# Kernel optimization log

Hardware: AMD Instinct MI355X
Metric: run time of the kernel (lower is better)

Reference implementation:

```python
import jax, jax.numpy as jnp
import numpy as np

N = 50000      # nodes
E = 800000     # edges
IN = 256       # in_dim
H = 3          # num_heads
C = 64         # hidden_dim (per head)
D = H * C      # per-layer width = 192
OUT = 64       # out_dim
EPS_BN = 1e-5


def _gat_layer(h, W, att_src, att_dst, bias, src, dst):
    """PyG GATConv (concat=True, no self loops, eval/no dropout).
    h: [N, F_in], W: [F_in, H*C], att_src/att_dst: [H, C], bias: [H*C]."""
    x = (h @ W).reshape(-1, H, C)                       # [N, H, C]
    a_s = jnp.einsum('nhc,hc->nh', x, att_src)          # [N, H]
    a_d = jnp.einsum('nhc,hc->nh', x, att_dst)          # [N, H]
    e = jax.nn.leaky_relu(a_s[src] + a_d[dst], 0.2)     # [E, H]
    # segment softmax over incoming edges of each destination node
    m = jax.ops.segment_max(e, dst, num_segments=N)     # [N, H]
    m = jnp.where(jnp.isfinite(m), m, 0.0)
    w = jnp.exp(e - m[dst])                             # [E, H]
    den = jax.ops.segment_sum(w, dst, num_segments=N)   # [N, H]
    alpha = w / (den[dst] + 1e-16)                      # [E, H]
    out = jax.ops.segment_sum(x[src] * alpha[:, :, None], dst, num_segments=N)
    return out.reshape(-1, D) + bias                    # [N, H*C]


def _batchnorm(h, gamma, beta):
    mu = h.mean(0)
    var = h.var(0)
    return (h - mu) * jax.lax.rsqrt(var + EPS_BN) * gamma + beta


def setup_inputs() -> dict:
    key = jax.random.key(0)
    ks = jax.random.split(key, 16)
    s_in = 1.0 / np.sqrt(IN)
    s_d = 1.0 / np.sqrt(D)
    inp = {
        'x': jax.random.normal(ks[0], (N, IN), jnp.float32),
        'W1': jax.random.normal(ks[1], (IN, D), jnp.float32) * s_in,
        'att_src1': jax.random.normal(ks[2], (H, C), jnp.float32) * s_d,
        'att_dst1': jax.random.normal(ks[3], (H, C), jnp.float32) * s_d,
        'b1': jnp.zeros((D,), jnp.float32),
        'g1': jnp.ones((D,), jnp.float32),
        'beta1': jnp.zeros((D,), jnp.float32),
        'W2': jax.random.normal(ks[4], (D, D), jnp.float32) * s_d,
        'att_src2': jax.random.normal(ks[5], (H, C), jnp.float32) * s_d,
        'att_dst2': jax.random.normal(ks[6], (H, C), jnp.float32) * s_d,
        'b2': jnp.zeros((D,), jnp.float32),
        'g2': jnp.ones((D,), jnp.float32),
        'beta2': jnp.zeros((D,), jnp.float32),
        'Wf': jax.random.normal(ks[7], (D, OUT), jnp.float32) * s_d,
        'bf': jnp.zeros((OUT,), jnp.float32),
        'edge_index': jax.random.randint(ks[8], (2, E), 0, N, jnp.int64),
    }
    return inp


def reference(x, W1, att_src1, att_dst1, b1, g1, beta1,
              W2, att_src2, att_dst2, b2, g2, beta2,
              Wf, bf, edge_index):
    src, dst = edge_index[0], edge_index[1]
    h1 = _gat_layer(x, W1, att_src1, att_dst1, b1, src, dst)
    h1 = _batchnorm(jax.nn.relu(h1), g1, beta1)
    h2 = _gat_layer(h1, W2, att_src2, att_dst2, b2, src, dst)
    h2 = _batchnorm(jax.nn.relu(h2), g2, beta2)
    h_sum = h1 + h2
    return h_sum @ Wf + bf
```

## Files before the change

kernel.cpp:

```cpp
#include <hip/hip_runtime.h>

#define NN 50000
#define NE 800000
#define DIN 256
#define NH 3
#define HC 64
#define DD 192
#define DF 64
#define NB 196

typedef __attribute__((ext_vector_type(8))) short s8bf;
typedef __attribute__((ext_vector_type(8))) unsigned short u16x8;
typedef __attribute__((ext_vector_type(4))) float f32x4;

__device__ __forceinline__ unsigned short f2bf(float f) {
    unsigned u = __float_as_uint(f);
    unsigned r = u + 0x7fffu + ((u >> 16) & 1u);
    return (unsigned short)(r >> 16);
}
__device__ __forceinline__ float bf2f(unsigned short h) {
    return __uint_as_float(((unsigned)h) << 16);
}
__device__ __forceinline__ void split2(float f, unsigned short& h, unsigned short& l) {
    h = f2bf(f);
    l = f2bf(f - bf2f(h));
}
__device__ __forceinline__ float rl_f(float v, int j) {
    return __int_as_float(__builtin_amdgcn_readlane(__float_as_int(v), j));
}

#define W1G (DIN / 8 * DD)
#define W2G (DD / 8 * DD)
#define WFG (DD / 8 * DF)
__global__ __launch_bounds__(256)
void wsplit_all(const float* __restrict__ W1, const float* __restrict__ W2,
                const float* __restrict__ Wf,
                unsigned short* __restrict__ W1hT, unsigned short* __restrict__ W1lT,
                unsigned short* __restrict__ W2hT, unsigned short* __restrict__ W2lT,
                unsigned short* __restrict__ WfhT, unsigned short* __restrict__ WflT) {
    int idx = blockIdx.x * 256 + threadIdx.x;
    const float* W; unsigned short *Wh, *Wl; int K, D, base;
    if (idx < W1G)                  { W = W1; Wh = W1hT; Wl = W1lT; K = DIN; D = DD; base = idx; }
    else if (idx < W1G + W2G)       { W = W2; Wh = W2hT; Wl = W2lT; K = DD;  D = DD; base = idx - W1G; }
    else if (idx < W1G + W2G + WFG) { W = Wf; Wh = WfhT; Wl = WflT; K = DD;  D = DF; base = idx - W1G - W2G; }
    else return;
    int kb = base / D, d = base - kb * D;
    u16x8 hv, lv;
#pragma unroll
    for (int q = 0; q < 8; ++q) {
        unsigned short h, l;
        split2(W[(size_t)(kb * 8 + q) * D + d], h, l);
        hv[q] = h; lv[q] = l;
    }
    *(u16x8*)(Wh + (size_t)d * K + kb * 8) = hv;
    *(u16x8*)(Wl + (size_t)d * K + kb * 8) = lv;
}

__global__ void bn_fin(const float* __restrict__ s1, const float* __restrict__ s2,
                       const float* __restrict__ g, const float* __restrict__ beta,
                       float* __restrict__ scale, float* __restrict__ shift) {
    int j = threadIdx.x;
    const float invn = 1.0f / NN;
    float mu = s1[j] * invn;
    float var = s2[j] * invn - mu * mu;
    float sc = g[j] * rsqrtf(var + 1e-5f);
    scale[j] = sc;
    shift[j] = beta[j] - mu * sc;
}

template<int K, int DOUT, int MODE, bool DOTS>
__global__ __launch_bounds__(256)
void mfma_gemm(const float* __restrict__ A1, const float* __restrict__ A2,
               const float* __restrict__ bb1, const float* __restrict__ sc1,
               const float* __restrict__ sh1,
               const float* __restrict__ bb2, const float* __restrict__ sc2,
               const float* __restrict__ sh2,
               const unsigned short* __restrict__ BhT, const unsigned short* __restrict__ BlT,
               const float* __restrict__ att_s, const float* __restrict__ att_d,
               float4* __restrict__ as4o, float4* __restrict__ ad4o,
               const float* __restrict__ obias, float* __restrict__ Yf,
               unsigned short* __restrict__ Yb, int n) {
    constexpr int NT = DOUT / 64;
    constexpr int KB8 = K / 8;
    __shared__ unsigned short AH[64 * KB8 * 8];
    __shared__ float sdots[DOTS ? 4 : 1][64][6];

    const int tid = threadIdx.x;
    const int wave = tid >> 6, lane = tid & 63;
    const int r = lane & 15, kg = lane >> 4;
    const int row0 = blockIdx.x * 64;
    const int col0 = wave * (DOUT / 4);

    for (int idx = tid; idx < 64 * KB8; idx += 256) {
        int row = idx / KB8, kb = idx - row * KB8;
        int grow = min(row0 + row, n - 1);
        int j = kb * 8;
        const float* ap = A1 + (size_t)grow * K + j;
        float v[8];
        *(float4*)&v[0] = *(const float4*)ap;
        *(float4*)&v[4] = *(const float4*)(ap + 4);
        if constexpr (MODE >= 1) {
#pragma unroll
            for (int q = 0; q < 8; ++q)
                v[q] = fmaxf(v[q] + bb1[j + q], 0.f) * sc1[j + q] + sh1[j + q];
        }
        if constexpr (MODE == 2) {
            const float* ap2 = A2 + (size_t)grow * K + j;
            float u[8];
            *(float4*)&u[0] = *(const float4*)ap2;
            *(float4*)&u[4] = *(const float4*)(ap2 + 4);
#pragma unroll
            for (int q = 0; q < 8; ++q)
                v[q] += fmaxf(u[q] + bb2[j + q], 0.f) * sc2[j + q] + sh2[j + q];
        }
        u16x8 hv;
#pragma unroll
        for (int q = 0; q < 8; ++q)
            hv[q] = f2bf(v[q]);
        int sw = kb ^ (row & 7);
        *(u16x8*)&AH[(row * KB8 + sw) * 8] = hv;
    }
    __syncthreads();

    int boff[NT];
#pragma unroll
    for (int t = 0; t < NT; ++t)
        boff[t] = (col0 + t * 16 + r) * K + kg * 8;

    f32x4 acc[4][NT] = {};

    for (int k0 = 0; k0 < K; k0 += 32) {
        s8bf bh[NT], bl[NT];
#pragma unroll
        for (int t = 0; t < NT; ++t) {
            bh[t] = *(const s8bf*)(BhT + boff[t] + k0);
            bl[t] = *(const s8bf*)(BlT + boff[t] + k0);
        }
        const int kb = k0 / 8 + kg;
        s8bf ah[4];
#pragma unroll
        for (int g = 0; g < 4; ++g) {
            int row = g * 16 + r;
            int sw = kb ^ (row & 7);
            ah[g] = *(const s8bf*)&AH[(row * KB8 + sw) * 8];
        }
#pragma unroll
        for (int g = 0; g < 4; ++g)
#pragma unroll
            for (int t = 0; t < NT; ++t) {
                acc[g][t] = __builtin_amdgcn_mfma_f32_16x16x32_bf16(ah[g], bh[t], acc[g][t], 0, 0, 0);
                acc[g][t] = __builtin_amdgcn_mfma_f32_16x16x32_bf16(ah[g], bl[t], acc[g][t], 0, 0, 0);
            }
    }

#pragma unroll
    for (int t = 0; t < NT; ++t) {
        int col = col0 + t * 16 + r;
        float b = (MODE == 2) ? obias[col] : 0.f;
#pragma unroll
        for (int g = 0; g < 4; ++g) {
#pragma unroll
            for (int rr = 0; rr < 4; ++rr) {
                int row = row0 + g * 16 + kg * 4 + rr;
                if (row < n) {
                    if constexpr (MODE == 2)
                        Yf[(size_t)row * DOUT + col] = acc[g][t][rr] + b;
                    else
                        Yb[(size_t)row * DOUT + col] = f2bf(acc[g][t][rr]);
                }
            }
        }
    }

    if constexpr (DOTS) {
        float asv[NT], adv[NT];
        int headt[NT];
#pragma unroll
        for (int t = 0; t < NT; ++t) {
            int col = col0 + t * 16 + r;
            asv[t] = att_s[col];
            adv[t] = att_d[col];
            headt[t] = (col0 + t * 16) >> 6;
        }
#pragma unroll
        for (int g = 0; g < 4; ++g) {
#pragma unroll
            for (int rr = 0; rr < 4; ++rr) {
                float rs0 = 0.f, rs1 = 0.f, rs2 = 0.f;
                float rd0 = 0.f, rd1 = 0.f, rd2 = 0.f;
#pragma unroll
                for (int t = 0; t < NT; ++t) {
                    float v = acc[g][t][rr];
                    float s = v * asv[t], dd = v * adv[t];
                    if (headt[t] == 0)      { rs0 += s; rd0 += dd; }
                    else if (headt[t] == 1) { rs1 += s; rd1 += dd; }
                    else                    { rs2 += s; rd2 += dd; }
                }
#pragma unroll
                for (int m = 1; m < 16; m <<= 1) {
                    rs0 += __shfl_xor(rs0, m); rs1 += __shfl_xor(rs1, m); rs2 += __shfl_xor(rs2, m);
                    rd0 += __shfl_xor(rd0, m); rd1 += __shfl_xor(rd1, m); rd2 += __shfl_xor(rd2, m);
                }
                if (r == 0) {
                    int row = g * 16 + kg * 4 + rr;
                    sdots[wave][row][0] = rs0; sdots[wave][row][1] = rs1; sdots[wave][row][2] = rs2;
                    sdots[wave][row][3] = rd0; sdots[wave][row][4] = rd1; sdots[wave][row][5] = rd2;
                }
            }
        }
        __syncthreads();
        if (tid < 64) {
            int row = row0 + tid;
            if (row < n) {
                float s0 = 0.f, s1 = 0.f, s2 = 0.f, d0 = 0.f, d1 = 0.f, d2 = 0.f;
#pragma unroll
                for (int w = 0; w < 4; ++w) {
                    s0 += sdots[w][tid][0]; s1 += sdots[w][tid][1]; s2 += sdots[w][tid][2];
                    d0 += sdots[w][tid][3]; d1 += sdots[w][tid][4]; d2 += sdots[w][tid][5];
                }
                as4o[row] = make_float4(s0, s1, s2, 0.f);
                ad4o[row] = make_float4(d0, d1, d2, 0.f);
            }
        }
    }
}

__global__ void hist_kernel(const int* __restrict__ dst, int* __restrict__ deg, int ne) {
    int e = blockIdx.x * blockDim.x + threadIdx.x;
    if (e < ne) atomicAdd(&deg[dst[e]], 1);
}

__global__ __launch_bounds__(256)
void blocksum_kernel(const int* __restrict__ deg, int* __restrict__ bsum) {
    int i = blockIdx.x * 256 + threadIdx.x;
    int v = (i < NN) ? deg[i] : 0;
#pragma unroll
    for (int off = 32; off; off >>= 1) v += __shfl_down(v, off);
    __shared__ int ws[4];
    if ((threadIdx.x & 63) == 0) ws[threadIdx.x >> 6] = v;
    __syncthreads();
    if (threadIdx.x == 0) bsum[blockIdx.x] = ws[0] + ws[1] + ws[2] + ws[3];
}

__global__ __launch_bounds__(256)
void scan_bsums(const int* __restrict__ bsum, int* __restrict__ boff,
                int* __restrict__ rowptr) {
    __shared__ int s[256];
    int t = threadIdx.x;
    int v = (t < NB) ? bsum[t] : 0;
    s[t] = v;
    __syncthreads();
    for (int off = 1; off < 256; off <<= 1) {
        int u = (t >= off) ? s[t - off] : 0;
        __syncthreads();
        s[t] += u;
        __syncthreads();
    }
    if (t < NB) boff[t] = s[t] - v;
    if (t == 255) rowptr[NN] = s[255];
}

__global__ __launch_bounds__(256)
void expand_kernel(const int* __restrict__ deg, const int* __restrict__ boff,
                   int* __restrict__ rowptr, int* __restrict__ cursor) {
    __shared__ int s[256];
    int t = threadIdx.x;
    int i = blockIdx.x * 256 + t;
    int v = (i < NN) ? deg[i] : 0;
    s[t] = v;
    __syncthreads();
    for (int off = 1; off < 256; off <<= 1) {
        int u = (t >= off) ? s[t - off] : 0;
        __syncthreads();
        s[t] += u;
        __syncthreads();
    }
    if (i < NN) {
        int excl = s[t] - v + boff[blockIdx.x];
        rowptr[i] = excl;
        cursor[i] = excl;
    }
}

__global__ void scatter_kernel(const int* __restrict__ src, const int* __restrict__ dst,
                               int* __restrict__ cursor, int* __restrict__ csr_src, int ne) {
    int e = blockIdx.x * blockDim.x + threadIdx.x;
    if (e >= ne) return;
    int d = dst[e];
    int pos = atomicAdd(&cursor[d], 1);
    csr_src[pos] = src[e];
}

__global__ __launch_bounds__(256)
void gat_gather(const unsigned short* __restrict__ xf,
                const float4* __restrict__ as4, const float4* __restrict__ ad4,
                const int* __restrict__ rowptr, const int* __restrict__ csr_src,
                float* __restrict__ outp) {
    int d = blockIdx.x * 4 + (threadIdx.x >> 6);
    if (d >= NN) return;
    const int lane = threadIdx.x & 63;
    const int beg = rowptr[d], end = rowptr[d + 1];
    const float4 adv = ad4[d];

    float a0 = 0.f, a1 = 0.f, a2 = 0.f;
    float den0 = 0.f, den1 = 0.f, den2 = 0.f;

    for (int base = beg; base < end; base += 64) {
        const int nb = min(64, end - base);
        int sl = 0;
        float w0 = 0.f, w1 = 0.f, w2 = 0.f;
        if (lane < nb) {
            sl = csr_src[base + lane];
            float4 av = as4[sl];
            float e0 = av.x + adv.x;
            float e1 = av.y + adv.y;
            float e2 = av.z + adv.z;
            e0 = e0 > 0.f ? e0 : 0.2f * e0;
            e1 = e1 > 0.f ? e1 : 0.2f * e1;
            e2 = e2 > 0.f ? e2 : 0.2f * e2;
            w0 = __expf(e0); w1 = __expf(e1); w2 = __expf(e2);
        }
        float r0 = w0, r1 = w1, r2 = w2;
#pragma unroll
        for (int off = 1; off < 64; off <<= 1) {
            r0 += __shfl_xor(r0, off);
            r1 += __shfl_xor(r1, off);
            r2 += __shfl_xor(r2, off);
        }
        den0 += r0; den1 += r1; den2 += r2;

        int j = 0;
        for (; j + 8 <= nb; j += 8) {
            const unsigned short* xp[8];
            float uw0[8], uw1[8], uw2[8];
#pragma unroll
            for (int k = 0; k < 8; ++k) {
                int s = __builtin_amdgcn_readlane(sl, j + k);
                xp[k] = xf + (size_t)s * DD;
                uw0[k] = rl_f(w0, j + k);
                uw1[k] = rl_f(w1, j + k);
                uw2[k] = rl_f(w2, j + k);
            }
            unsigned short f0[8], f1[8], f2[8];
#pragma unroll
            for (int k = 0; k < 8; ++k) {
                f0[k] = xp[k][lane];
                f1[k] = xp[k][64 + lane];
                f2[k] = xp[k][128 + lane];
            }
#pragma unroll
            for (int k = 0; k < 8; ++k) {
                a0 = fmaf(bf2f(f0[k]), uw0[k], a0);
                a1 = fmaf(bf2f(f1[k]), uw1[k], a1);
                a2 = fmaf(bf2f(f2[k]), uw2[k], a2);
            }
        }
        for (; j < nb; ++j) {
            int s = __builtin_amdgcn_readlane(sl, j);
            float u0 = rl_f(w0, j), u1 = rl_f(w1, j), u2 = rl_f(w2, j);
            const unsigned short* xp = xf + (size_t)s * DD;
            a0 = fmaf(bf2f(xp[lane]),       u0, a0);
            a1 = fmaf(bf2f(xp[64 + lane]),  u1, a1);
            a2 = fmaf(bf2f(xp[128 + lane]), u2, a2);
        }
    }
    size_t o = (size_t)d * DD + lane;
    outp[o]       = a0 / (den0 + 1e-16f);
    outp[o + 64]  = a1 / (den1 + 1e-16f);
    outp[o + 128] = a2 / (den2 + 1e-16f);
}

__global__ __launch_bounds__(192)
void bn_stats(const float* __restrict__ hbuf, const float* __restrict__ bias,
              float* __restrict__ s1, float* __restrict__ s2, int n) {
    int j = threadIdx.x;
    float b = bias[j];
    int r0 = blockIdx.x * 64;
    int r1 = min(r0 + 64, n);
    float a = 0.f, q = 0.f;
    for (int r = r0; r < r1; ++r) {
        float v = hbuf[(size_t)r * DD + j] + b;
        v = fmaxf(v, 0.f);
        a += v; q += v * v;
    }
    atomicAdd(&s1[j], a);
    atomicAdd(&s2[j], q);
}

extern "C" void kernel_launch(void* const* d_in, const int* in_sizes, int n_in,
                              void* d_out, int out_size, void* d_ws, size_t ws_size,
                              hipStream_t stream) {
    const float* x   = (const float*)d_in[0];
    const float* W1  = (const float*)d_in[1];
    const float* as1 = (const float*)d_in[2];
    const float* ad1 = (const float*)d_in[3];
    const float* b1  = (const float*)d_in[4];
    const float* g1  = (const float*)d_in[5];
    const float* be1 = (const float*)d_in[6];
    const float* W2  = (const float*)d_in[7];
    const float* as2 = (const float*)d_in[8];
    const float* ad2 = (const float*)d_in[9];
    const float* b2  = (const float*)d_in[10];
    const float* g2  = (const float*)d_in[11];
    const float* be2 = (const float*)d_in[12];
    const float* Wf  = (const float*)d_in[13];
    const float* bf  = (const float*)d_in[14];
    const int*   ei  = (const int*)d_in[15];
    const int* src = ei;
    const int* dst = ei + NE;
    float* out = (float*)d_out;

    float* ws = (float*)d_ws;
    float* CB1 = ws;
    float* CB2 = CB1 + (size_t)NN * DD;
    float4* AS4 = (float4*)(CB2 + (size_t)NN * DD);
    float4* AD4 = AS4 + NN;
    int* DEG   = (int*)(AD4 + NN);
    float* S1a = (float*)(DEG + NN);
    float* S2a = S1a + DD;
    float* S1b = S2a + DD;
    float* S2b = S1b + DD;
    float* SC1 = S2b + DD;
    float* SH1 = SC1 + DD;
    float* SC2 = SH1 + DD;
    float* SH2 = SC2 + DD;
    int* ROWPTR = (int*)(SH2 + DD);
    int* CURSOR = ROWPTR + NN + 1;
    int* BSUM   = CURSOR + NN;
    int* BOFF   = BSUM + NB;
    int* CSRS   = BOFF + NB;
    unsigned short* R    = (unsigned short*)(CSRS + NE);
    unsigned short* Abf  = R;
    unsigned short* W1hT = Abf + (size_t)NN * DD;
    unsigned short* W1lT = W1hT + DIN * DD;
    unsigned short* W2hT = W1lT + DIN * DD;
    unsigned short* W2lT = W2hT + DD * DD;
    unsigned short* WfhT = W2lT + DD * DD;
    unsigned short* WflT = WfhT + DD * DF;

    const int edge_grid = (NE + 255) / 256;
    const int gemm_grid = (NN + 63) / 64;
    const int gat_grid  = (NN + 3) / 4;
    const int bns_grid  = (NN + 63) / 64;
    const int wsp_grid  = (W1G + W2G + WFG + 255) / 256;

    hipMemsetAsync(DEG, 0, (size_t)NN * 4 + 4 * DD * 4, stream);

    hist_kernel<<<edge_grid, 256, 0, stream>>>(dst, DEG, NE);
    blocksum_kernel<<<NB, 256, 0, stream>>>(DEG, BSUM);
    scan_bsums<<<1, 256, 0, stream>>>(BSUM, BOFF, ROWPTR);
    expand_kernel<<<NB, 256, 0, stream>>>(DEG, BOFF, ROWPTR, CURSOR);
    scatter_kernel<<<edge_grid, 256, 0, stream>>>(src, dst, CURSOR, CSRS, NE);

    wsplit_all<<<wsp_grid, 256, 0, stream>>>(W1, W2, Wf, W1hT, W1lT, W2hT, W2lT, WfhT, WflT);

    mfma_gemm<DIN, DD, 0, true><<<gemm_grid, 256, 0, stream>>>(
        x, nullptr,
        nullptr, nullptr, nullptr,
        nullptr, nullptr, nullptr,
        W1hT, W1lT, as1, ad1, AS4, AD4, nullptr, nullptr, Abf, NN);
    gat_gather<<<gat_grid, 256, 0, stream>>>(Abf, AS4, AD4, ROWPTR, CSRS, CB1);
    bn_stats<<<bns_grid, 192, 0, stream>>>(CB1, b1, S1a, S2a, NN);
    bn_fin<<<1, DD, 0, stream>>>(S1a, S2a, g1, be1, SC1, SH1);

    mfma_gemm<DD, DD, 1, true><<<gemm_grid, 256, 0, stream>>>(
        CB1, nullptr,
        b1, SC1, SH1,
        nullptr, nullptr, nullptr,
        W2hT, W2lT, as2, ad2, AS4, AD4, nullptr, nullptr, Abf, NN);
    gat_gather<<<gat_grid, 256, 0, stream>>>(Abf, AS4, AD4, ROWPTR, CSRS, CB2);
    bn_stats<<<bns_grid, 192, 0, stream>>>(CB2, b2, S1b, S2b, NN);
    bn_fin<<<1, DD, 0, stream>>>(S1b, S2b, g2, be2, SC2, SH2);

    mfma_gemm<DD, DF, 2, false><<<gemm_grid, 256, 0, stream>>>(
        CB1, CB2,
        b1, SC1, SH1,
        b2, SC2, SH2,
        WfhT, WflT, nullptr, nullptr, nullptr, nullptr, bf, out, nullptr, NN);
}
```

Baseline: 417.2 us.

## Fold BN finalize into GEMM prologue and software-pipeline A/B loads

Removes the two single-block bn_fin launches by having each GEMM block compute the batchnorm scale and shift from the raw sums into shared memory. The A-tile staging loop and the MFMA k-loop are software-pipelined so the next iteration's global and LDS loads are issued before the current compute. This cuts launch overhead and hides load latency, at the cost of redundant per-block BN math and higher register pressure.

```diff
diff --git a/kernel.cpp b/kernel.cpp
--- a/kernel.cpp
+++ b/kernel.cpp
@@ -56,25 +56,15 @@
     *(u16x8*)(Wl + (size_t)d * K + kb * 8) = lv;
 }
 
-__global__ void bn_fin(const float* __restrict__ s1, const float* __restrict__ s2,
-                       const float* __restrict__ g, const float* __restrict__ beta,
-                       float* __restrict__ scale, float* __restrict__ shift) {
-    int j = threadIdx.x;
-    const float invn = 1.0f / NN;
-    float mu = s1[j] * invn;
-    float var = s2[j] * invn - mu * mu;
-    float sc = g[j] * rsqrtf(var + 1e-5f);
-    scale[j] = sc;
-    shift[j] = beta[j] - mu * sc;
-}
-
 template<int K, int DOUT, int MODE, bool DOTS>
 __global__ __launch_bounds__(256)
 void mfma_gemm(const float* __restrict__ A1, const float* __restrict__ A2,
-               const float* __restrict__ bb1, const float* __restrict__ sc1,
-               const float* __restrict__ sh1,
-               const float* __restrict__ bb2, const float* __restrict__ sc2,
-               const float* __restrict__ sh2,
+               const float* __restrict__ bb1, const float* __restrict__ S1a_,
+               const float* __restrict__ S2a_, const float* __restrict__ g1_,
+               const float* __restrict__ be1_,
+               const float* __restrict__ bb2, const float* __restrict__ S1b_,
+               const float* __restrict__ S2b_, const float* __restrict__ g2_,
+               const float* __restrict__ be2_,
                const unsigned short* __restrict__ BhT, const unsigned short* __restrict__ BlT,
                const float* __restrict__ att_s, const float* __restrict__ att_d,
                float4* __restrict__ as4o, float4* __restrict__ ad4o,
@@ -82,8 +72,10 @@
                unsigned short* __restrict__ Yb, int n) {
     constexpr int NT = DOUT / 64;
     constexpr int KB8 = K / 8;
+    constexpr int NCF = (MODE == 2) ? 4 : (MODE == 1 ? 2 : 1);
     __shared__ unsigned short AH[64 * KB8 * 8];
     __shared__ float sdots[DOTS ? 4 : 1][64][6];
+    __shared__ float cf[NCF][DD];
 
     const int tid = threadIdx.x;
     const int wave = tid >> 6, lane = tid & 63;
@@ -91,27 +83,70 @@
     const int row0 = blockIdx.x * 64;
     const int col0 = wave * (DOUT / 4);
 
-    for (int idx = tid; idx < 64 * KB8; idx += 256) {
+    if constexpr (MODE >= 1) {
+        if (tid < DD) {
+            const float invn = 1.0f / NN;
+            float mu = S1a_[tid] * invn;
+            float var = S2a_[tid] * invn - mu * mu;
+            float sc = g1_[tid] * rsqrtf(var + 1e-5f);
+            cf[0][tid] = sc;
+            cf[1][tid] = be1_[tid] - mu * sc;
+            if constexpr (MODE == 2) {
+                mu = S1b_[tid] * invn;
+                var = S2b_[tid] * invn - mu * mu;
+                sc = g2_[tid] * rsqrtf(var + 1e-5f);
+                cf[2][tid] = sc;
+                cf[3][tid] = be2_[tid] - mu * sc;
+            }
+        }
+        __syncthreads();
+    }
+
+    constexpr int SIT = 64 * KB8 / 256;
+    auto aoff = [&](int i) {
+        int idx = tid + i * 256;
         int row = idx / KB8, kb = idx - row * KB8;
         int grow = min(row0 + row, n - 1);
+        return (size_t)grow * K + kb * 8;
+    };
+    float4 cv0, cv1, cu0, cu1;
+    {
+        size_t o0 = aoff(0);
+        cv0 = *(const float4*)(A1 + o0);
+        cv1 = *(const float4*)(A1 + o0 + 4);
+        if constexpr (MODE == 2) {
+            cu0 = *(const float4*)(A2 + o0);
+            cu1 = *(const float4*)(A2 + o0 + 4);
+        }
+    }
+#pragma unroll
+    for (int i = 0; i < SIT; ++i) {
+        float4 nv0, nv1, nu0, nu1;
+        if (i + 1 < SIT) {
+            size_t on = aoff(i + 1);
+            nv0 = *(const float4*)(A1 + on);
+            nv1 = *(const float4*)(A1 + on + 4);
+            if constexpr (MODE == 2) {
+                nu0 = *(const float4*)(A2 + on);
+                nu1 = *(const float4*)(A2 + on + 4);
+            }
+        }
+        int idx = tid + i * 256;
+        int row = idx / KB8, kb = idx - row * KB8;
         int j = kb * 8;
-        const float* ap = A1 + (size_t)grow * K + j;
         float v[8];
-        *(float4*)&v[0] = *(const float4*)ap;
-        *(float4*)&v[4] = *(const float4*)(ap + 4);
+        *(float4*)&v[0] = cv0; *(float4*)&v[4] = cv1;
         if constexpr (MODE >= 1) {
 #pragma unroll
             for (int q = 0; q < 8; ++q)
-                v[q] = fmaxf(v[q] + bb1[j + q], 0.f) * sc1[j + q] + sh1[j + q];
+                v[q] = fmaxf(v[q] + bb1[j + q], 0.f) * cf[0][j + q] + cf[1][j + q];
         }
         if constexpr (MODE == 2) {
-            const float* ap2 = A2 + (size_t)grow * K + j;
             float u[8];
-            *(float4*)&u[0] = *(const float4*)ap2;
-            *(float4*)&u[4] = *(const float4*)(ap2 + 4);
+            *(float4*)&u[0] = cu0; *(float4*)&u[4] = cu1;
 #pragma unroll
             for (int q = 0; q < 8; ++q)
-                v[q] += fmaxf(u[q] + bb2[j + q], 0.f) * sc2[j + q] + sh2[j + q];
+                v[q] += fmaxf(u[q] + bb2[j + q], 0.f) * cf[2][j + q] + cf[3][j + q];
         }
         u16x8 hv;
 #pragma unroll
@@ -119,6 +154,8 @@
             hv[q] = f2bf(v[q]);
         int sw = kb ^ (row & 7);
         *(u16x8*)&AH[(row * KB8 + sw) * 8] = hv;
+        cv0 = nv0; cv1 = nv1;
+        if constexpr (MODE == 2) { cu0 = nu0; cu1 = nu1; }
     }
     __syncthreads();
 
@@ -129,28 +166,44 @@
 
     f32x4 acc[4][NT] = {};
 
-    for (int k0 = 0; k0 < K; k0 += 32) {
-        s8bf bh[NT], bl[NT];
+    auto loadB = [&](int k0, s8bf* bh, s8bf* bl) {
 #pragma unroll
         for (int t = 0; t < NT; ++t) {
             bh[t] = *(const s8bf*)(BhT + boff[t] + k0);
             bl[t] = *(const s8bf*)(BlT + boff[t] + k0);
         }
+    };
+    auto loadA = [&](int k0, s8bf* ah) {
         const int kb = k0 / 8 + kg;
-        s8bf ah[4];
 #pragma unroll
         for (int g = 0; g < 4; ++g) {
             int row = g * 16 + r;
             int sw = kb ^ (row & 7);
             ah[g] = *(const s8bf*)&AH[(row * KB8 + sw) * 8];
         }
+    };
+
+    s8bf bh[NT], bl[NT], ah4[4];
+    loadB(0, bh, bl);
+    loadA(0, ah4);
+#pragma unroll
+    for (int k0 = 0; k0 < K; k0 += 32) {
+        s8bf nbh[NT], nbl[NT], nah[4];
+        if (k0 + 32 < K) {
+            loadB(k0 + 32, nbh, nbl);
+            loadA(k0 + 32, nah);
+        }
 #pragma unroll
         for (int g = 0; g < 4; ++g)
 #pragma unroll
             for (int t = 0; t < NT; ++t) {
-                acc[g][t] = __builtin_amdgcn_mfma_f32_16x16x32_bf16(ah[g], bh[t], acc[g][t], 0, 0, 0);
-                acc[g][t] = __builtin_amdgcn_mfma_f32_16x16x32_bf16(ah[g], bl[t], acc[g][t], 0, 0, 0);
-            }
+                acc[g][t] = __builtin_amdgcn_mfma_f32_16x16x32_bf16(ah4[g], bh[t], acc[g][t], 0, 0, 0);
+                acc[g][t] = __builtin_amdgcn_mfma_f32_16x16x32_bf16(ah4[g], bl[t], acc[g][t], 0, 0, 0);
+            }
+#pragma unroll
+        for (int t = 0; t < NT; ++t) { bh[t] = nbh[t]; bl[t] = nbl[t]; }
+#pragma unroll
+        for (int g = 0; g < 4; ++g) ah4[g] = nah[g];
     }
 
 #pragma unroll
@@ -456,25 +509,23 @@
 
     mfma_gemm<DIN, DD, 0, true><<<gemm_grid, 256, 0, stream>>>(
         x, nullptr,
-        nullptr, nullptr, nullptr,
-        nullptr, nullptr, nullptr,
+        nullptr, nullptr, nullptr, nullptr, nullptr,
+        nullptr, nullptr, nullptr, nullptr, nullptr,
         W1hT, W1lT, as1, ad1, AS4, AD4, nullptr, nullptr, Abf, NN);
     gat_gather<<<gat_grid, 256, 0, stream>>>(Abf, AS4, AD4, ROWPTR, CSRS, CB1);
     bn_stats<<<bns_grid, 192, 0, stream>>>(CB1, b1, S1a, S2a, NN);
-    bn_fin<<<1, DD, 0, stream>>>(S1a, S2a, g1, be1, SC1, SH1);
 
     mfma_gemm<DD, DD, 1, true><<<gemm_grid, 256, 0, stream>>>(
         CB1, nullptr,
-        b1, SC1, SH1,
-        nullptr, nullptr, nullptr,
+        b1, S1a, S2a, g1, be1,
+        nullptr, nullptr, nullptr, nullptr, nullptr,
         W2hT, W2lT, as2, ad2, AS4, AD4, nullptr, nullptr, Abf, NN);
     gat_gather<<<gat_grid, 256, 0, stream>>>(Abf, AS4, AD4, ROWPTR, CSRS, CB2);
     bn_stats<<<bns_grid, 192, 0, stream>>>(CB2, b2, S1b, S2b, NN);
-    bn_fin<<<1, DD, 0, stream>>>(S1b, S2b, g2, be2, SC2, SH2);
 
     mfma_gemm<DD, DF, 2, false><<<gemm_grid, 256, 0, stream>>>(
         CB1, CB2,
-        b1, SC1, SH1,
-        b2, SC2, SH2,
+        b1, S1a, S2a, g1, be1,
+        b2, S1b, S2b, g2, be2,
         WfhT, WflT, nullptr, nullptr, nullptr, nullptr, bf, out, nullptr, NN);
 }
```

New measurement: 405.5 us, median of 2. -2.8%, faster.
